# Performance work log

Hardware: AMD Instinct MI355X
Metric: run time of the kernel (lower is better)

Reference implementation:

```python
import jax, jax.numpy as jnp
import numpy as np

N_STEP = 3
N_INP = 256


def setup_inputs() -> dict:
    key = jax.random.key(0)
    ks = jax.random.split(key, 8)
    bs, L, n = 16, 128, N_INP
    s = 1.0 / np.sqrt(n)
    s2 = 1.0 / np.sqrt(2 * n)
    feat = jax.random.normal(ks[0], (bs, L, n), dtype=jnp.float32)
    mask = jnp.ones((bs, L), dtype=jnp.float32)
    # stacked per-step Linear params (torch Linear: y = x @ W.T + b)
    aggW = jax.random.uniform(ks[1], (N_STEP, n, n), minval=-s, maxval=s, dtype=jnp.float32)
    aggB = jax.random.uniform(ks[2], (N_STEP, n), minval=-s, maxval=s, dtype=jnp.float32)
    attnW = jax.random.uniform(ks[3], (N_STEP, n, 2 * n), minval=-s2, maxval=s2, dtype=jnp.float32)
    attnB = jax.random.uniform(ks[4], (N_STEP, n), minval=-s2, maxval=s2, dtype=jnp.float32)
    updW = jax.random.uniform(ks[5], (N_STEP, n, 2 * n), minval=-s2, maxval=s2, dtype=jnp.float32)
    updB = jax.random.uniform(ks[6], (N_STEP, n), minval=-s2, maxval=s2, dtype=jnp.float32)
    return {"feat": feat, "mask": mask, "aggW": aggW, "aggB": aggB,
            "attnW": attnW, "attnB": attnB, "updW": updW, "updB": updB}


def reference(feat, mask, aggW, aggB, attnW, attnB, updW, updB):
    bs, L, n = feat.shape
    hid = feat
    for i in range(N_STEP):
        hid = hid * mask[:, :, None]
        x = hid @ aggW[i].T + aggB[i]  # [b, s, n]
        # attn Linear on concat(x_s, x_j) splits into two matmuls
        W1 = attnW[i][:, :n]   # acts on x_s (sequence position)
        W2 = attnW[i][:, n:]   # acts on x_j (query node)
        p = x @ W1.T           # [b, s, n]
        q = x @ W2.T           # [b, j, n]
        # logits[b, j, s, c] = p[b, s, c] + q[b, j, c] + bias[c]
        logits = p[:, None, :, :] + q[:, :, None, :] + attnB[i]
        w = jax.nn.softmax(logits, axis=2)  # softmax over sequence dim per channel
        agg = jax.nn.sigmoid(jnp.einsum('bjsn,bsn->bjn', w, x))
        cat = jnp.concatenate([x, agg], axis=-1)  # [b, s, 2n]; dropout is identity (eval)
        hid = cat @ updW[i].T + updB[i]
    return hid
```

## Files before the change

### kernel.cpp

```cpp
#include <hip/hip_runtime.h>
#include <hip/hip_fp16.h>

#define NBLK  128
#define NPACK 192
#define NT    512
#define FPAD  16

typedef _Float16 h2_t  __attribute__((ext_vector_type(2)));
typedef _Float16 half8 __attribute__((ext_vector_type(8)));
typedef float    f32x4 __attribute__((ext_vector_type(4)));

#define AG_LD(p)    __hip_atomic_load((p), __ATOMIC_RELAXED, __HIP_MEMORY_SCOPE_AGENT)
#define AG_ST(p, v) __hip_atomic_store((p), (v), __ATOMIC_RELAXED, __HIP_MEMORY_SCOPE_AGENT)

__device__ __forceinline__ unsigned pkh(float a, float b) {
    const __half2 h = __floats2half2_rn(a, b);
    return __builtin_bit_cast(unsigned, h);
}
__device__ __forceinline__ float fdot2(unsigned w, unsigned a, float c) {
#if __has_builtin(__builtin_amdgcn_fdot2)
    return __builtin_amdgcn_fdot2(__builtin_bit_cast(h2_t, w),
                                  __builtin_bit_cast(h2_t, a), c, false);
#else
    const float2 fw = __half22float2(__builtin_bit_cast(__half2, w));
    const float2 fa = __half22float2(__builtin_bit_cast(__half2, a));
    return c + fw.x * fa.x + fw.y * fa.y;
#endif
}

__device__ __forceinline__ half8 ldw(const unsigned* p) {
    return __builtin_bit_cast(half8, *(const uint4*)p);
}
__device__ __forceinline__ f32x4 MF(half8 a, half8 b, f32x4 c) {
    return __builtin_amdgcn_mfma_f32_16x16x32_f16(a, b, c, 0, 0, 0);
}

__device__ __forceinline__ void bar_arrive(int n, unsigned* flags, int lid) {
    __syncthreads();
    if (threadIdx.x == 0)
        __hip_atomic_store(&flags[lid * FPAD], (unsigned)n, __ATOMIC_RELEASE,
                           __HIP_MEMORY_SCOPE_AGENT);
}
__device__ __forceinline__ void bar_wait_batch(int n, unsigned* flags, int b) {
    if (threadIdx.x < 8) {
        while ((int)__hip_atomic_load(&flags[(b * 8 + threadIdx.x) * FPAD],
                                      __ATOMIC_RELAXED,
                                      __HIP_MEMORY_SCOPE_AGENT) < n)
            __builtin_amdgcn_s_sleep(1);
    }
    __syncthreads();
}


__global__ __launch_bounds__(NT, 2) void pack_k(
    const float* __restrict__ aggW, const float* __restrict__ attnW,
    const float* __restrict__ updW, unsigned* __restrict__ WtH,
    unsigned* __restrict__ flags)
{
    __shared__ float Tl[64][65];
    const int bb = blockIdx.x, tid = threadIdx.x;
    const int m = bb >> 4, t = bb & 15, tr = t >> 2, tc = t & 3;
    const float* src; int stride, off;
    if (m < 3)      { src = aggW  + (size_t)m * 65536;        stride = 256; off = 0;   }
    else if (m < 6) { src = attnW + (size_t)(m - 3) * 131072; stride = 512; off = 0;   }
    else if (m < 9) { src = updW  + (size_t)(m - 6) * 131072; stride = 512; off = 0;   }
    else            { src = updW  + (size_t)(m - 9) * 131072; stride = 512; off = 256; }
    unsigned* dstu = WtH + (size_t)m * 32768;
    #pragma unroll
    for (int it = 0; it < 2; ++it) {
        const int j = it * 512 + tid, row = j >> 4, q = (j & 15) * 4;
        const float4 v = *(const float4*)(src + (size_t)(tr * 64 + row) * stride + off + tc * 64 + q);
        Tl[row][q + 0] = v.x; Tl[row][q + 1] = v.y;
        Tl[row][q + 2] = v.z; Tl[row][q + 3] = v.w;
    }
    if (bb == 0)
        for (int z = tid; z < 256 * FPAD; z += NT) flags[z] = 0u;
    __syncthreads();
    #pragma unroll
    for (int it = 0; it < 4; ++it) {
        const int j = it * 512 + tid, cl = j >> 5, pr = j & 31;
        const unsigned val = pkh(Tl[cl][pr * 2], Tl[cl][pr * 2 + 1]);
        const int C = tr * 64 + cl, P = tc * 32 + pr;
        size_t idx;
        if (m < 9) {
            const int ttn = C >> 4, lc = C & 15;
            const int kc = P >> 4, g = (P >> 2) & 3, sl = P & 3;
            idx = (size_t)((ttn * 8 + kc) * 256 + (g * 16 + lc) * 4 + sl);
        } else {
            idx = (size_t)(P >> 2) * 1024 + (size_t)C * 4 + (P & 3);
        }
        dstu[idx] = val;
    }
}

__device__ __forceinline__ float phaseB(int i, int b, int c, int rq, int tid,
                                        const float* __restrict__ part,
                                        const unsigned* __restrict__ WtH,
                                        const float* __restrict__ updB,
                                        float* S, unsigned* aggh, uint4* buf) {
    const float* pbase = part + (size_t)((i & 1) * 128 + b * 8 + rq * 4) * 768;
    float m[4], d[4], nn[4];
    #pragma unroll
    for (int j = 0; j < 4; ++j) {
        const float* pp = pbase + (size_t)j * 768;
        m[j]  = AG_LD(pp + c);
        d[j]  = AG_LD(pp + 256 + c);
        nn[j] = AG_LD(pp + 512 + c);
    }
    #pragma unroll
    for (int st = 1; st < 4; st <<= 1) {
        #pragma unroll
        for (int j = 0; j < 4; j += 2 * st) {
            const float Mn = fmaxf(m[j], m[j + st]);
            const float sa = __expf(m[j] - Mn), sb = __expf(m[j + st] - Mn);
            d[j]  = d[j] * sa + d[j + st] * sb;
            nn[j] = nn[j] * sa + nn[j + st] * sb;
            m[j]  = Mn;
        }
    }
    S[rq * 256 + c] = m[0];
    S[512 + rq * 256 + c] = d[0];
    S[1024 + rq * 256 + c] = nn[0];
    __syncthreads();
    if (tid < 128) {
        float sg[2];
        #pragma unroll
        for (int u = 0; u < 2; ++u) {
            const int cc = 2 * tid + u;
            const float m0 = S[cc], m1 = S[256 + cc];
            const float Mx = fmaxf(m0, m1);
            const float s0 = __expf(m0 - Mx), s1 = __expf(m1 - Mx);
            const float dd = S[512 + cc] * s0 + S[768 + cc] * s1;
            const float nv = S[1024 + cc] * s0 + S[1280 + cc] * s1;
            sg[u] = 1.f / (1.f + __expf(-(nv / dd)));
        }
        aggh[tid] = pkh(sg[0], sg[1]);
    }
    __syncthreads();
    const unsigned* Uq = WtH + (size_t)(9 + i) * 32768;
    const int g0 = rq * 16;
    float a0 = 0.f, a1 = 0.f, a2 = 0.f, a3 = 0.f;
    #pragma unroll
    for (int ph = 0; ph < 2; ++ph) {
        #pragma unroll
        for (int j = 0; j < 8; ++j) {
            const uint4 w = buf[j];
            if (ph < 1)
                buf[j] = *(const uint4*)(Uq + (size_t)(g0 + 8 + j) * 1024 + c * 4);
            const uint4 a = *(const uint4*)&aggh[(g0 + ph * 8 + j) * 4];
            a0 = fdot2(w.x, a.x, a0);
            a1 = fdot2(w.y, a.y, a1);
            a2 = fdot2(w.z, a.z, a2);
            a3 = fdot2(w.w, a.w, a3);
        }
    }
    const float au = (a0 + a1) + (a2 + a3);
    S[rq * 256 + c] = au;
    __syncthreads();
    return S[c] + S[256 + c] + updB[i * 256 + c];
}

__global__ __launch_bounds__(NT, 2) void main_k(
    const float* __restrict__ feat,
    const float* __restrict__ mask,
    const float* __restrict__ aggB,
    const float* __restrict__ updB,
    const unsigned* __restrict__ WtH,
    float* __restrict__ part,
    unsigned* flags,
    float* __restrict__ out)
{
    __shared__ __align__(16) float ldsf[6160];
    unsigned* hid_uu = (unsigned*)ldsf;
    unsigned* x_uu   = (unsigned*)ldsf + 2112;
    float*    accl   = ldsf + 4224;
    float*    S      = ldsf + 4480;
    unsigned* aggh   = (unsigned*)ldsf + 6016;
    float*    msk    = ldsf + 6144;

    const int bid = blockIdx.x;
    const int tid = threadIdx.x;
    const int c   = tid & 255;
    const int rq  = tid >> 8;
    const int wid = tid >> 6, lane = tid & 63;
    const int lr  = lane & 15, lg = lane >> 4;
    const int b   = 2 * (bid & 7) + ((bid >> 3) & 1);
    const int jj  = bid >> 4;
    const int lid = b * 8 + jj;
    const int row0 = b * 128 + jj * 16;

    #pragma unroll
    for (int it = 0; it < 4; ++it) {
        const int j = it * 512 + tid, r = j >> 7, pr = j & 127;
        const float2 f = *(const float2*)(feat + (size_t)(row0 + r) * 256 + pr * 2);
        const float mv = mask[row0 + r];
        hid_uu[r * 132 + pr] = pkh(f.x * mv, f.y * mv);
    }
    if (tid < 16) msk[tid] = mask[row0 + tid];
    __syncthreads();

    const int ct0 = wid * 2, ct1 = wid * 2 + 1;

    f32x4 xu0 = {}, xu1 = {};
    uint4 u2buf[8];

    for (int i = 0; i < 3; ++i) {
        if (i > 0) {
            const float accU = phaseB(i - 1, b, c, rq, tid, part, WtH, updB,
                                      S, aggh, u2buf);
            if (rq == 0) accl[c] = accU;
            __syncthreads();
            #pragma unroll
            for (int tt = 0; tt < 2; ++tt) {
                const int t = wid * 2 + tt;
                const f32x4 xa = tt ? xu1 : xu0;
                const float av = accl[t * 16 + lr];
                float hv[4], pv[4];
                #pragma unroll
                for (int q = 0; q < 4; ++q)
                    hv[q] = (xa[q] + av) * msk[lg * 4 + q];
                #pragma unroll
                for (int q = 0; q < 4; ++q) pv[q] = __shfl_xor(hv[q], 1);
                if (!(lr & 1)) {
                    const int p2 = t * 8 + (lr >> 1);
                    #pragma unroll
                    for (int q = 0; q < 4; ++q)
                        hid_uu[(lg * 4 + q) * 132 + p2] = pkh(hv[q], pv[q]);
                }
            }
            __syncthreads();
        }

        f32x4 xr0, xr1;

        {
            const unsigned* W0 = WtH + (size_t)i * 32768;
            half8 a[8];
            #pragma unroll
            for (int kc = 0; kc < 8; ++kc)
                a[kc] = ldw(hid_uu + lr * 132 + kc * 16 + lg * 4);
            #pragma unroll
            for (int tt = 0; tt < 2; ++tt) {
                const int t = wid * 2 + tt;
                f32x4 acc = {};
                #pragma unroll
                for (int kc = 0; kc < 8; ++kc)
                    acc = MF(a[kc], ldw(W0 + (size_t)(t * 8 + kc) * 256 + lane * 4), acc);
                const float bb = aggB[i * 256 + t * 16 + lr];
                #pragma unroll
                for (int q = 0; q < 4; ++q) acc[q] += bb;
                if (tt) xr1 = acc; else xr0 = acc;
                float pv[4];
                #pragma unroll
                for (int q = 0; q < 4; ++q) pv[q] = __shfl_xor(acc[q], 1);
                if (!(lr & 1)) {
                    const int p2 = t * 8 + (lr >> 1);
                    #pragma unroll
                    for (int q = 0; q < 4; ++q)
                        x_uu[(lg * 4 + q) * 132 + p2] = pkh(acc[q], pv[q]);
                }
            }
            __syncthreads();
        }

        {
            const unsigned* W1 = WtH + (size_t)(3 + i) * 32768;
            const unsigned* U1 = WtH + (size_t)(6 + i) * 32768;
            half8 a2[8];
            #pragma unroll
            for (int kc = 0; kc < 8; ++kc)
                a2[kc] = ldw(x_uu + lr * 132 + kc * 16 + lg * 4);
            float* pb = part + (size_t)((i & 1) * 128 + lid) * 768;
            #pragma unroll
            for (int tt = 0; tt < 2; ++tt) {
                const int t = wid * 2 + tt;
                f32x4 acc = {};
                #pragma unroll
                for (int kc = 0; kc < 8; ++kc)
                    acc = MF(a2[kc], ldw(W1 + (size_t)(t * 8 + kc) * 256 + lane * 4), acc);
                const f32x4 xa = tt ? xr1 : xr0;
                float m4 = fmaxf(fmaxf(acc[0], acc[1]), fmaxf(acc[2], acc[3]));
                m4 = fmaxf(m4, __shfl_xor(m4, 16));
                const float m16 = fmaxf(m4, __shfl_xor(m4, 32));
                float d4 = 0.f, n4 = 0.f;
                #pragma unroll
                for (int q = 0; q < 4; ++q) {
                    const float e = __expf(acc[q] - m16);
                    d4 += e;
                    n4 += e * xa[q];
                }
                d4 += __shfl_xor(d4, 16); d4 += __shfl_xor(d4, 32);
                n4 += __shfl_xor(n4, 16); n4 += __shfl_xor(n4, 32);
                if (lg == 0) {
                    const int cc = t * 16 + lr;
                    AG_ST(pb + cc, m16);
                    AG_ST(pb + 256 + cc, d4);
                    AG_ST(pb + 512 + cc, n4);
                }
            }
            bar_arrive(i + 1, flags, lid);
            #pragma unroll
            for (int tt = 0; tt < 2; ++tt) {
                const int t = wid * 2 + tt;
                f32x4 acc = {};
                #pragma unroll
                for (int kc = 0; kc < 8; ++kc)
                    acc = MF(a2[kc], ldw(U1 + (size_t)(t * 8 + kc) * 256 + lane * 4), acc);
                if (tt) xu1 = acc; else xu0 = acc;
            }
            {
                const unsigned* Uq = WtH + (size_t)(9 + i) * 32768;
                #pragma unroll
                for (int j = 0; j < 8; ++j)
                    u2buf[j] = *(const uint4*)(Uq + (size_t)(rq * 16 + j) * 1024 + c * 4);
            }
            bar_wait_batch(i + 1, flags, b);
        }
    }

    {
        const float accU = phaseB(2, b, c, rq, tid, part, WtH, updB, S, aggh, u2buf);
        if (rq == 0) accl[c] = accU;
        __syncthreads();
        #pragma unroll
        for (int tt = 0; tt < 2; ++tt) {
            const int t = wid * 2 + tt;
            const f32x4 xa = tt ? xu1 : xu0;
            const float av = accl[t * 16 + lr];
            #pragma unroll
            for (int q = 0; q < 4; ++q)
                out[(size_t)(row0 + lg * 4 + q) * 256 + t * 16 + lr] = xa[q] + av;
        }
    }
}

extern "C" void kernel_launch(void* const* d_in, const int* in_sizes, int n_in,
                              void* d_out, int out_size, void* d_ws, size_t ws_size,
                              hipStream_t stream) {
    const float* feat  = (const float*)d_in[0];
    const float* mask  = (const float*)d_in[1];
    const float* aggW  = (const float*)d_in[2];
    const float* aggB  = (const float*)d_in[3];
    const float* attnW = (const float*)d_in[4];
    const float* updW  = (const float*)d_in[6];
    const float* updB  = (const float*)d_in[7];

    unsigned* WtH = (unsigned*)d_ws;
    float* part = (float*)(WtH + 12 * 32768);
    unsigned* flags = (unsigned*)(part + 2 * 256 * 768);

    pack_k<<<NPACK, NT, 0, stream>>>(aggW, attnW, updW, WtH, flags);
    main_k<<<NBLK, NT, 0, stream>>>(feat, mask, aggB, updB, WtH, part, flags,
                                    (float*)d_out);
}
```

Baseline: 105.0 us.

## Prefetch next matmul's weights into registers across GEMM stages

```diff
diff --git a/kernel.cpp b/kernel.cpp
--- a/kernel.cpp
+++ b/kernel.cpp
@@ -30,6 +30,9 @@
 
 __device__ __forceinline__ half8 ldw(const unsigned* p) {
     return __builtin_bit_cast(half8, *(const uint4*)p);
+}
+__device__ __forceinline__ half8 h8(uint4 w) {
+    return __builtin_bit_cast(half8, w);
 }
 __device__ __forceinline__ f32x4 MF(half8 a, half8 b, f32x4 c) {
     return __builtin_amdgcn_mfma_f32_16x16x32_f16(a, b, c, 0, 0, 0);
@@ -160,7 +163,7 @@
     return S[c] + S[256 + c] + updB[i * 256 + c];
 }
 
-__global__ __launch_bounds__(NT, 2) void main_k(
+__global__ __launch_bounds__(NT, 1) void main_k(
     const float* __restrict__ feat,
     const float* __restrict__ mask,
     const float* __restrict__ aggB,
@@ -197,9 +200,12 @@
         hid_uu[r * 132 + pr] = pkh(f.x * mv, f.y * mv);
     }
     if (tid < 16) msk[tid] = mask[row0 + tid];
-    __syncthreads();
-
-    const int ct0 = wid * 2, ct1 = wid * 2 + 1;
+
+    uint4 wb[16];
+    #pragma unroll
+    for (int j = 0; j < 16; ++j)
+        wb[j] = *(const uint4*)(WtH + (size_t)(wid * 16 + j) * 256 + lane * 4);
+    __syncthreads();
 
     f32x4 xu0 = {}, xu1 = {};
     uint4 u2buf[8];
@@ -234,7 +240,7 @@
         f32x4 xr0, xr1;
 
         {
-            const unsigned* W0 = WtH + (size_t)i * 32768;
+            const unsigned* W1 = WtH + (size_t)(3 + i) * 32768;
             half8 a[8];
             #pragma unroll
             for (int kc = 0; kc < 8; ++kc)
@@ -244,8 +250,12 @@
                 const int t = wid * 2 + tt;
                 f32x4 acc = {};
                 #pragma unroll
-                for (int kc = 0; kc < 8; ++kc)
-                    acc = MF(a[kc], ldw(W0 + (size_t)(t * 8 + kc) * 256 + lane * 4), acc);
+                for (int kc = 0; kc < 8; ++kc) {
+                    const int j = tt * 8 + kc;
+                    const uint4 w = wb[j];
+                    wb[j] = *(const uint4*)(W1 + (size_t)(wid * 16 + j) * 256 + lane * 4);
+                    acc = MF(a[kc], h8(w), acc);
+                }
                 const float bb = aggB[i * 256 + t * 16 + lr];
                 #pragma unroll
                 for (int q = 0; q < 4; ++q) acc[q] += bb;
@@ -264,8 +274,8 @@
         }
 
         {
-            const unsigned* W1 = WtH + (size_t)(3 + i) * 32768;
             const unsigned* U1 = WtH + (size_t)(6 + i) * 32768;
+            const unsigned* Wn = WtH + (size_t)(i == 2 ? 0 : i + 1) * 32768;
             half8 a2[8];
             #pragma unroll
             for (int kc = 0; kc < 8; ++kc)
@@ -276,8 +286,12 @@
                 const int t = wid * 2 + tt;
                 f32x4 acc = {};
                 #pragma unroll
-                for (int kc = 0; kc < 8; ++kc)
-                    acc = MF(a2[kc], ldw(W1 + (size_t)(t * 8 + kc) * 256 + lane * 4), acc);
+                for (int kc = 0; kc < 8; ++kc) {
+                    const int j = tt * 8 + kc;
+                    const uint4 w = wb[j];
+                    wb[j] = *(const uint4*)(U1 + (size_t)(wid * 16 + j) * 256 + lane * 4);
+                    acc = MF(a2[kc], h8(w), acc);
+                }
                 const f32x4 xa = tt ? xr1 : xr0;
                 float m4 = fmaxf(fmaxf(acc[0], acc[1]), fmaxf(acc[2], acc[3]));
                 m4 = fmaxf(m4, __shfl_xor(m4, 16));
@@ -301,11 +315,14 @@
             bar_arrive(i + 1, flags, lid);
             #pragma unroll
             for (int tt = 0; tt < 2; ++tt) {
-                const int t = wid * 2 + tt;
                 f32x4 acc = {};
                 #pragma unroll
-                for (int kc = 0; kc < 8; ++kc)
-                    acc = MF(a2[kc], ldw(U1 + (size_t)(t * 8 + kc) * 256 + lane * 4), acc);
+                for (int kc = 0; kc < 8; ++kc) {
+                    const int j = tt * 8 + kc;
+                    const uint4 w = wb[j];
+                    wb[j] = *(const uint4*)(Wn + (size_t)(wid * 16 + j) * 256 + lane * 4);
+                    acc = MF(a2[kc], h8(w), acc);
+                }
                 if (tt) xu1 = acc; else xu0 = acc;
             }
             {
```

Measured after the change: 108.4 us. +3.2%, slower.
